# Kernel optimization log

Measured on AMD Instinct MI355X. Metric: run time of the kernel, lower is better.

The kernel has to match this reference:

```python
import jax, jax.numpy as jnp
import numpy as np

N = 100000      # num nodes
E = 1600000     # num edges (avg degree 16)
IN = 128        # input_dim
D = 32          # output_dim per head
H = 4           # heads
ALPHA = 0.2     # LeakyReLU slope


def setup_inputs() -> dict:
    key = jax.random.key(0)
    k1, k2, k3, k4, k5 = jax.random.split(key, 5)
    X = jax.random.normal(k1, (N, IN), dtype=jnp.float32)
    # fc weights, xavier-like scale (bias=False in the module)
    W0 = jax.random.normal(k2, (H * D, IN), dtype=jnp.float32) * (1.0 / np.sqrt(IN))
    W1 = jax.random.normal(k3, (H * D, IN), dtype=jnp.float32) * (1.0 / np.sqrt(IN))
    a0 = jax.random.normal(k4, (H, 1, D), dtype=jnp.float32) * (1.0 / np.sqrt(D))
    deg = E // N
    # CSR rows expanded to sorted segment ids: every node has exactly `deg` out-edges
    edge_src = jnp.repeat(jnp.arange(N, dtype=jnp.int32), deg)
    column_index = jax.random.randint(k5, (E,), 0, N, dtype=jnp.int32)
    return {"X": X, "W0": W0, "W1": W1, "a0": a0,
            "edge_src": edge_src, "column_index": column_index}


def _leaky_relu(x):
    return jnp.where(x > 0, x, ALPHA * x)


def reference(X, W0, W1, a0, edge_src, column_index):
    # Linear projections, split per head: [H, N, D]
    X0 = _leaky_relu(X @ W0.T).reshape(N, H, D).transpose(1, 0, 2)
    X1 = _leaky_relu(X @ W1.T).reshape(N, H, D).transpose(1, 0, 2)
    a = a0[:, 0, :]                                    # [H, D]
    # SDDMM: att[h,e] = a[h] . (X0[h,src(e)] + X1[h,dst(e)])
    s0 = jnp.einsum('hnd,hd->hn', X0, a)               # [H, N]
    s1 = jnp.einsum('hnd,hd->hn', X1, a)
    att = s0[:, edge_src] + s1[:, column_index]        # [H, E]
    # per-head global min-max normalization, then exp (module's softmax surrogate)
    mx = jnp.max(att, axis=1, keepdims=True)
    mn = jnp.min(att, axis=1, keepdims=True)
    att = jnp.exp((att - mn) / (mx - mn))
    # sparse row-sum (softmax denominator): [N, H]
    rows_sum = jax.ops.segment_sum(att.T, edge_src, num_segments=N)
    # SpMM: aggregate neighbor features weighted by att -> [N, H, D]
    msg = att.T[:, :, None] * X1[:, column_index, :].transpose(1, 0, 2)  # [E, H, D]
    h_prime = jax.ops.segment_sum(msg, edge_src, num_segments=N)
    return h_prime / rows_sum[:, :, None]
```

## Files before the change

kernel.cpp:

```cpp
#include <hip/hip_runtime.h>
#include <hip/hip_bf16.h>
#include <stdint.h>

#define NN 100000
#define EE 1600000
#define ALPHA 0.2f
#define MM_BLOCKS 1563

typedef __bf16 bf16_t;
typedef __bf16 bf16x8 __attribute__((ext_vector_type(8)));
typedef __bf16 bf16x4 __attribute__((ext_vector_type(4)));
typedef float fx4 __attribute__((ext_vector_type(4)));


__global__ __launch_bounds__(512) void wconv_kernel(
    const float* __restrict__ W0, const float* __restrict__ W1,
    uint4* __restrict__ Wtab)
{
  const int task = blockIdx.x * 512 + threadIdx.x;
  if (task >= 4096) return;
  const int sct = task >> 8, sks = (task >> 6) & 3, sl = task & 63;
  const int r  = sct * 16 + (sl & 15);
  const int c0 = (sks * 4 + (sl >> 4)) * 8;
  const float* src = (r < 128 ? W0 + (size_t)r * 128 : W1 + (size_t)(r - 128) * 128) + c0;
  const fx4 wa = *(const fx4*)src;
  const fx4 wb = *(const fx4*)(src + 4);
  bf16x8 wf;
  wf[0] = (bf16_t)wa[0]; wf[1] = (bf16_t)wa[1];
  wf[2] = (bf16_t)wa[2]; wf[3] = (bf16_t)wa[3];
  wf[4] = (bf16_t)wb[0]; wf[5] = (bf16_t)wb[1];
  wf[6] = (bf16_t)wb[2]; wf[7] = (bf16_t)wb[3];
  Wtab[task] = __builtin_bit_cast(uint4, wf);
}

#define GEMM_BLOCKS 391
__global__ __launch_bounds__(512) void gemm_kernel(
    const float* __restrict__ X, const uint4* __restrict__ Wtab,
    const float* __restrict__ a0,
    bf16_t* __restrict__ F1, float* __restrict__ s0g, float* __restrict__ s1g)
{
  __shared__ uint4 lw[4096];
  const int tid  = threadIdx.x;
  const int wv   = tid >> 6;
  const int lane = tid & 63;
  const int col  = lane & 15;
  const int quad = lane >> 4;

#pragma unroll
  for (int i = 0; i < 8; ++i) {
    const int task = i * 512 + tid;
    __builtin_amdgcn_global_load_lds(
        (const __attribute__((address_space(1))) uint32_t*)(Wtab + task),
        (__attribute__((address_space(3))) uint32_t*)(&lw[task]), 16, 0, 0);
  }
  __syncthreads();

#pragma unroll 1
  for (int tt = 0; tt < 2; ++tt) {
    const int tile = blockIdx.x * 8 + wv + tt * (GEMM_BLOCKS * 8);
    if (tile >= (NN / 16)) continue;
    const int n0   = tile * 16;
    const int node = n0 + col;

    fx4 acc[16];
#pragma unroll
    for (int c = 0; c < 16; ++c) {
      acc[c][0] = 0.f; acc[c][1] = 0.f; acc[c][2] = 0.f; acc[c][3] = 0.f;
    }

    const float* xrow = X + (size_t)node * 128 + quad * 8;
#pragma unroll
    for (int ks = 0; ks < 4; ++ks) {
      fx4 xa = *(const fx4*)(xrow + ks * 32);
      fx4 xb = *(const fx4*)(xrow + ks * 32 + 4);
      bf16x8 xf;
      xf[0] = (bf16_t)xa[0]; xf[1] = (bf16_t)xa[1];
      xf[2] = (bf16_t)xa[2]; xf[3] = (bf16_t)xa[3];
      xf[4] = (bf16_t)xb[0]; xf[5] = (bf16_t)xb[1];
      xf[6] = (bf16_t)xb[2]; xf[7] = (bf16_t)xb[3];
#pragma unroll
      for (int ct = 0; ct < 16; ++ct) {
        const uint4 w4 = lw[(ct * 4 + ks) * 64 + lane];
        const bf16x8 wf = __builtin_bit_cast(bf16x8, w4);
        acc[ct] = __builtin_amdgcn_mfma_f32_16x16x32_bf16(wf, xf, acc[ct], 0, 0, 0);
      }
    }

    float sdot[8];
#pragma unroll
    for (int s = 0; s < 8; ++s) sdot[s] = 0.f;

#pragma unroll
    for (int ct = 0; ct < 16; ++ct) {
      const fx4 av = *(const fx4*)(a0 + (ct & 7) * 16 + quad * 4);
#pragma unroll
      for (int r = 0; r < 4; ++r) {
        float v = acc[ct][r];
        v = v > 0.f ? v : ALPHA * v;
        acc[ct][r] = v;
        sdot[ct >> 1] += v * av[r];
      }
      if (ct >= 8) {
        bf16x4 p;
        p[0] = (bf16_t)acc[ct][0]; p[1] = (bf16_t)acc[ct][1];
        p[2] = (bf16_t)acc[ct][2]; p[3] = (bf16_t)acc[ct][3];
        *(bf16x4*)(F1 + (size_t)node * 128 + (ct - 8) * 16 + quad * 4) = p;
      }
    }

#pragma unroll
    for (int s = 0; s < 8; ++s) {
      sdot[s] += __shfl_xor(sdot[s], 16);
      sdot[s] += __shfl_xor(sdot[s], 32);
    }
    if (quad == 0) {
      fx4 r0, r1;
      r0[0] = sdot[0]; r0[1] = sdot[1]; r0[2] = sdot[2]; r0[3] = sdot[3];
      r1[0] = sdot[4]; r1[1] = sdot[5]; r1[2] = sdot[6]; r1[3] = sdot[7];
      *(fx4*)(s0g + (size_t)node * 4) = r0;
      *(fx4*)(s1g + (size_t)node * 4) = r1;
    }
  }
}

__global__ __launch_bounds__(256) void minmax1_kernel(
    const int* __restrict__ cidx, const float* __restrict__ s0g,
    const float* __restrict__ s1g, float* __restrict__ partial)
{
  __shared__ float s_red[4][8];
  const int t = blockIdx.x * 256 + threadIdx.x;
  fx4 mx, mn;
#pragma unroll
  for (int h = 0; h < 4; ++h) { mx[h] = -1e30f; mn[h] = 1e30f; }
  if (t < EE / 4) {
    const int node = t >> 2;
    const fx4 s0v = *(const fx4*)(s0g + (size_t)node * 4);
    const int4 c4 = ((const int4*)cidx)[t];
    const int cc[4] = {c4.x, c4.y, c4.z, c4.w};
#pragma unroll
    for (int j = 0; j < 4; ++j) {
      const fx4 s1v = *(const fx4*)(s1g + (size_t)cc[j] * 4);
#pragma unroll
      for (int h = 0; h < 4; ++h) {
        const float att = s0v[h] + s1v[h];
        mx[h] = fmaxf(mx[h], att);
        mn[h] = fminf(mn[h], att);
      }
    }
  }
#pragma unroll
  for (int off = 1; off < 64; off <<= 1) {
#pragma unroll
    for (int h = 0; h < 4; ++h) {
      mx[h] = fmaxf(mx[h], __shfl_xor(mx[h], off));
      mn[h] = fminf(mn[h], __shfl_xor(mn[h], off));
    }
  }
  const int wv = threadIdx.x >> 6;
  if ((threadIdx.x & 63) == 0) {
#pragma unroll
    for (int h = 0; h < 4; ++h) {
      s_red[wv][h] = mx[h];
      s_red[wv][4 + h] = mn[h];
    }
  }
  __syncthreads();
  if (threadIdx.x < 8) {
    const int s = threadIdx.x;
    float v = s_red[0][s];
    if (s < 4) { v = fmaxf(v, s_red[1][s]); v = fmaxf(v, s_red[2][s]); v = fmaxf(v, s_red[3][s]); }
    else       { v = fminf(v, s_red[1][s]); v = fminf(v, s_red[2][s]); v = fminf(v, s_red[3][s]); }
    partial[blockIdx.x * 8 + s] = v;
  }
}

__global__ __launch_bounds__(256) void minmax2_kernel(
    const float* __restrict__ partial, float* __restrict__ mm)
{
  __shared__ float s_red[4][8];
  fx4 mx, mn;
#pragma unroll
  for (int h = 0; h < 4; ++h) { mx[h] = -1e30f; mn[h] = 1e30f; }
  for (int g = threadIdx.x; g < MM_BLOCKS; g += 256) {
    const fx4 p0 = *(const fx4*)(partial + g * 8);
    const fx4 p1 = *(const fx4*)(partial + g * 8 + 4);
#pragma unroll
    for (int h = 0; h < 4; ++h) {
      mx[h] = fmaxf(mx[h], p0[h]);
      mn[h] = fminf(mn[h], p1[h]);
    }
  }
#pragma unroll
  for (int off = 1; off < 64; off <<= 1) {
#pragma unroll
    for (int h = 0; h < 4; ++h) {
      mx[h] = fmaxf(mx[h], __shfl_xor(mx[h], off));
      mn[h] = fminf(mn[h], __shfl_xor(mn[h], off));
    }
  }
  const int wv = threadIdx.x >> 6;
  if ((threadIdx.x & 63) == 0) {
#pragma unroll
    for (int h = 0; h < 4; ++h) {
      s_red[wv][h] = mx[h];
      s_red[wv][4 + h] = mn[h];
    }
  }
  __syncthreads();
  if (threadIdx.x < 8) {
    const int s = threadIdx.x;
    float v = s_red[0][s];
    if (s < 4) { v = fmaxf(v, s_red[1][s]); v = fmaxf(v, s_red[2][s]); v = fmaxf(v, s_red[3][s]); }
    else       { v = fminf(v, s_red[1][s]); v = fminf(v, s_red[2][s]); v = fminf(v, s_red[3][s]); }
    mm[s] = v;
  }
}

__global__ __launch_bounds__(256) void aggregate_kernel(
    const int* __restrict__ cidx, const float* __restrict__ s0g,
    const float* __restrict__ s1g, const bf16_t* __restrict__ F1,
    const float* __restrict__ mm, float* __restrict__ out)
{
  const int t = blockIdx.x * 256 + threadIdx.x;
  const int node = t >> 4;
  if (node >= NN) return;
  const int sub = t & 15;
  const int h = sub >> 2;
  const float mxv = mm[h];
  const float mnv = mm[4 + h];
  const float scale = 1.f / (mxv - mnv);
  const float s0v = s0g[node * 4 + h];
  float a_[8] = {0.f, 0.f, 0.f, 0.f, 0.f, 0.f, 0.f, 0.f};
  float wsum = 0.f;

  const int4* ce4 = (const int4*)(cidx + (size_t)node * 16);
  const int4 c01 = ce4[0], c23 = ce4[1], c45 = ce4[2], c67 = ce4[3];
  const int cc[16] = {c01.x, c01.y, c01.z, c01.w, c23.x, c23.y, c23.z, c23.w,
                      c45.x, c45.y, c45.z, c45.w, c67.x, c67.y, c67.z, c67.w};

  float s1v[16];
  bf16x8 f[16];
#pragma unroll
  for (int j = 0; j < 16; ++j) {
    const int c = cc[j];
    s1v[j] = s1g[(size_t)c * 4 + h];
    f[j] = *(const bf16x8*)(F1 + (size_t)c * 128 + sub * 8);
  }
  __builtin_amdgcn_sched_barrier(0);

#pragma unroll
  for (int j = 0; j < 16; ++j) {
    const float w = __expf((s0v + s1v[j] - mnv) * scale);
    wsum += w;
#pragma unroll
    for (int k = 0; k < 8; ++k) a_[k] += w * (float)f[j][k];
  }

  const float inv = 1.f / wsum;
  fx4 r0, r1;
#pragma unroll
  for (int j = 0; j < 4; ++j) { r0[j] = a_[j] * inv; r1[j] = a_[4 + j] * inv; }
  float* op = out + (size_t)node * 128 + sub * 8;
  *(fx4*)op = r0;
  *(fx4*)(op + 4) = r1;
}

extern "C" void kernel_launch(void* const* d_in, const int* in_sizes, int n_in,
                              void* d_out, int out_size, void* d_ws, size_t ws_size,
                              hipStream_t stream)
{
  const float* X   = (const float*)d_in[0];
  const float* W0  = (const float*)d_in[1];
  const float* W1  = (const float*)d_in[2];
  const float* a0  = (const float*)d_in[3];
  const int* cidx  = (const int*)d_in[5];
  char* ws = (char*)d_ws;
  uint4*    Wtab    = (uint4*)ws;
  bf16_t*   F1      = (bf16_t*)(ws + 65536);
  float*    s0g     = (float*)(ws + 25665536);
  float*    s1g     = (float*)(ws + 27265536);
  float*    mm      = (float*)(ws + 28865536);
  float*    partial = (float*)(ws + 28865600);
  float*    out     = (float*)d_out;

  wconv_kernel<<<8, 512, 0, stream>>>(W0, W1, Wtab);
  gemm_kernel<<<GEMM_BLOCKS, 512, 0, stream>>>(X, Wtab, a0, F1, s0g, s1g);
  minmax1_kernel<<<MM_BLOCKS, 256, 0, stream>>>(cidx, s0g, s1g, partial);
  minmax2_kernel<<<1, 256, 0, stream>>>(partial, mm);
  aggregate_kernel<<<6250, 256, 0, stream>>>(cidx, s0g, s1g, F1, mm, out);
}
```

Measured before the change: 212.2 us.

## Fold final min-max reduction into aggregate kernel and drop minmax2 launch

Removes the single-block minmax2 kernel. Each aggregate block now redundantly reduces the 391 per-block partials into shared memory before doing its own work. The first-stage min-max kernel uses 1024-thread blocks, so there are fewer partials to reduce. The GEMM kernel launches 782 blocks with one tile per wave instead of looping twice over tiles. The aim is to cut a serial single-block launch and its dependency bubble, at the cost of 6250 blocks each re-reading about 12 KB of partials.

```diff
diff --git a/kernel.cpp b/kernel.cpp
--- a/kernel.cpp
+++ b/kernel.cpp
@@ -5,7 +5,7 @@
 #define NN 100000
 #define EE 1600000
 #define ALPHA 0.2f
-#define MM_BLOCKS 1563
+#define MM1_BLOCKS 391
 
 typedef __bf16 bf16_t;
 typedef __bf16 bf16x8 __attribute__((ext_vector_type(8)));
@@ -33,7 +33,6 @@
   Wtab[task] = __builtin_bit_cast(uint4, wf);
 }
 
-#define GEMM_BLOCKS 391
 __global__ __launch_bounds__(512) void gemm_kernel(
     const float* __restrict__ X, const uint4* __restrict__ Wtab,
     const float* __restrict__ a0,
@@ -55,80 +54,77 @@
   }
   __syncthreads();
 
-#pragma unroll 1
-  for (int tt = 0; tt < 2; ++tt) {
-    const int tile = blockIdx.x * 8 + wv + tt * (GEMM_BLOCKS * 8);
-    if (tile >= (NN / 16)) continue;
-    const int n0   = tile * 16;
-    const int node = n0 + col;
-
-    fx4 acc[16];
-#pragma unroll
-    for (int c = 0; c < 16; ++c) {
-      acc[c][0] = 0.f; acc[c][1] = 0.f; acc[c][2] = 0.f; acc[c][3] = 0.f;
-    }
-
-    const float* xrow = X + (size_t)node * 128 + quad * 8;
-#pragma unroll
-    for (int ks = 0; ks < 4; ++ks) {
-      fx4 xa = *(const fx4*)(xrow + ks * 32);
-      fx4 xb = *(const fx4*)(xrow + ks * 32 + 4);
-      bf16x8 xf;
-      xf[0] = (bf16_t)xa[0]; xf[1] = (bf16_t)xa[1];
-      xf[2] = (bf16_t)xa[2]; xf[3] = (bf16_t)xa[3];
-      xf[4] = (bf16_t)xb[0]; xf[5] = (bf16_t)xb[1];
-      xf[6] = (bf16_t)xb[2]; xf[7] = (bf16_t)xb[3];
-#pragma unroll
-      for (int ct = 0; ct < 16; ++ct) {
-        const uint4 w4 = lw[(ct * 4 + ks) * 64 + lane];
-        const bf16x8 wf = __builtin_bit_cast(bf16x8, w4);
-        acc[ct] = __builtin_amdgcn_mfma_f32_16x16x32_bf16(wf, xf, acc[ct], 0, 0, 0);
-      }
-    }
-
-    float sdot[8];
-#pragma unroll
-    for (int s = 0; s < 8; ++s) sdot[s] = 0.f;
-
+  const int tile = blockIdx.x * 8 + wv;
+  if (tile >= (NN / 16)) return;
+  const int n0   = tile * 16;
+  const int node = n0 + col;
+
+  fx4 acc[16];
+#pragma unroll
+  for (int c = 0; c < 16; ++c) {
+    acc[c][0] = 0.f; acc[c][1] = 0.f; acc[c][2] = 0.f; acc[c][3] = 0.f;
+  }
+
+  const float* xrow = X + (size_t)node * 128 + quad * 8;
+#pragma unroll
+  for (int ks = 0; ks < 4; ++ks) {
+    fx4 xa = *(const fx4*)(xrow + ks * 32);
+    fx4 xb = *(const fx4*)(xrow + ks * 32 + 4);
+    bf16x8 xf;
+    xf[0] = (bf16_t)xa[0]; xf[1] = (bf16_t)xa[1];
+    xf[2] = (bf16_t)xa[2]; xf[3] = (bf16_t)xa[3];
+    xf[4] = (bf16_t)xb[0]; xf[5] = (bf16_t)xb[1];
+    xf[6] = (bf16_t)xb[2]; xf[7] = (bf16_t)xb[3];
 #pragma unroll
     for (int ct = 0; ct < 16; ++ct) {
-      const fx4 av = *(const fx4*)(a0 + (ct & 7) * 16 + quad * 4);
-#pragma unroll
-      for (int r = 0; r < 4; ++r) {
-        float v = acc[ct][r];
-        v = v > 0.f ? v : ALPHA * v;
-        acc[ct][r] = v;
-        sdot[ct >> 1] += v * av[r];
-      }
-      if (ct >= 8) {
-        bf16x4 p;
-        p[0] = (bf16_t)acc[ct][0]; p[1] = (bf16_t)acc[ct][1];
-        p[2] = (bf16_t)acc[ct][2]; p[3] = (bf16_t)acc[ct][3];
-        *(bf16x4*)(F1 + (size_t)node * 128 + (ct - 8) * 16 + quad * 4) = p;
-      }
-    }
-
-#pragma unroll
-    for (int s = 0; s < 8; ++s) {
-      sdot[s] += __shfl_xor(sdot[s], 16);
-      sdot[s] += __shfl_xor(sdot[s], 32);
-    }
-    if (quad == 0) {
-      fx4 r0, r1;
-      r0[0] = sdot[0]; r0[1] = sdot[1]; r0[2] = sdot[2]; r0[3] = sdot[3];
-      r1[0] = sdot[4]; r1[1] = sdot[5]; r1[2] = sdot[6]; r1[3] = sdot[7];
-      *(fx4*)(s0g + (size_t)node * 4) = r0;
-      *(fx4*)(s1g + (size_t)node * 4) = r1;
-    }
-  }
-}
-
-__global__ __launch_bounds__(256) void minmax1_kernel(
+      const uint4 w4 = lw[(ct * 4 + ks) * 64 + lane];
+      const bf16x8 wf = __builtin_bit_cast(bf16x8, w4);
+      acc[ct] = __builtin_amdgcn_mfma_f32_16x16x32_bf16(wf, xf, acc[ct], 0, 0, 0);
+    }
+  }
+
+  float sdot[8];
+#pragma unroll
+  for (int s = 0; s < 8; ++s) sdot[s] = 0.f;
+
+#pragma unroll
+  for (int ct = 0; ct < 16; ++ct) {
+    const fx4 av = *(const fx4*)(a0 + (ct & 7) * 16 + quad * 4);
+#pragma unroll
+    for (int r = 0; r < 4; ++r) {
+      float v = acc[ct][r];
+      v = v > 0.f ? v : ALPHA * v;
+      acc[ct][r] = v;
+      sdot[ct >> 1] += v * av[r];
+    }
+    if (ct >= 8) {
+      bf16x4 p;
+      p[0] = (bf16_t)acc[ct][0]; p[1] = (bf16_t)acc[ct][1];
+      p[2] = (bf16_t)acc[ct][2]; p[3] = (bf16_t)acc[ct][3];
+      *(bf16x4*)(F1 + (size_t)node * 128 + (ct - 8) * 16 + quad * 4) = p;
+    }
+  }
+
+#pragma unroll
+  for (int s = 0; s < 8; ++s) {
+    sdot[s] += __shfl_xor(sdot[s], 16);
+    sdot[s] += __shfl_xor(sdot[s], 32);
+  }
+  if (quad == 0) {
+    fx4 r0, r1;
+    r0[0] = sdot[0]; r0[1] = sdot[1]; r0[2] = sdot[2]; r0[3] = sdot[3];
+    r1[0] = sdot[4]; r1[1] = sdot[5]; r1[2] = sdot[6]; r1[3] = sdot[7];
+    *(fx4*)(s0g + (size_t)node * 4) = r0;
+    *(fx4*)(s1g + (size_t)node * 4) = r1;
+  }
+}
+
+__global__ __launch_bounds__(1024) void minmax1_kernel(
     const int* __restrict__ cidx, const float* __restrict__ s0g,
     const float* __restrict__ s1g, float* __restrict__ partial)
 {
-  __shared__ float s_red[4][8];
-  const int t = blockIdx.x * 256 + threadIdx.x;
+  __shared__ float s_red[16][8];
+  const int t = blockIdx.x * 1024 + threadIdx.x;
   fx4 mx, mn;
 #pragma unroll
   for (int h = 0; h < 4; ++h) { mx[h] = -1e30f; mn[h] = 1e30f; }
@@ -168,66 +164,71 @@
   if (threadIdx.x < 8) {
     const int s = threadIdx.x;
     float v = s_red[0][s];
-    if (s < 4) { v = fmaxf(v, s_red[1][s]); v = fmaxf(v, s_red[2][s]); v = fmaxf(v, s_red[3][s]); }
-    else       { v = fminf(v, s_red[1][s]); v = fminf(v, s_red[2][s]); v = fminf(v, s_red[3][s]); }
+    if (s < 4) {
+#pragma unroll
+      for (int w = 1; w < 16; ++w) v = fmaxf(v, s_red[w][s]);
+    } else {
+#pragma unroll
+      for (int w = 1; w < 16; ++w) v = fminf(v, s_red[w][s]);
+    }
     partial[blockIdx.x * 8 + s] = v;
-  }
-}
-
-__global__ __launch_bounds__(256) void minmax2_kernel(
-    const float* __restrict__ partial, float* __restrict__ mm)
-{
-  __shared__ float s_red[4][8];
-  fx4 mx, mn;
-#pragma unroll
-  for (int h = 0; h < 4; ++h) { mx[h] = -1e30f; mn[h] = 1e30f; }
-  for (int g = threadIdx.x; g < MM_BLOCKS; g += 256) {
-    const fx4 p0 = *(const fx4*)(partial + g * 8);
-    const fx4 p1 = *(const fx4*)(partial + g * 8 + 4);
-#pragma unroll
-    for (int h = 0; h < 4; ++h) {
-      mx[h] = fmaxf(mx[h], p0[h]);
-      mn[h] = fminf(mn[h], p1[h]);
-    }
-  }
-#pragma unroll
-  for (int off = 1; off < 64; off <<= 1) {
-#pragma unroll
-    for (int h = 0; h < 4; ++h) {
-      mx[h] = fmaxf(mx[h], __shfl_xor(mx[h], off));
-      mn[h] = fminf(mn[h], __shfl_xor(mn[h], off));
-    }
-  }
-  const int wv = threadIdx.x >> 6;
-  if ((threadIdx.x & 63) == 0) {
-#pragma unroll
-    for (int h = 0; h < 4; ++h) {
-      s_red[wv][h] = mx[h];
-      s_red[wv][4 + h] = mn[h];
-    }
-  }
-  __syncthreads();
-  if (threadIdx.x < 8) {
-    const int s = threadIdx.x;
-    float v = s_red[0][s];
-    if (s < 4) { v = fmaxf(v, s_red[1][s]); v = fmaxf(v, s_red[2][s]); v = fmaxf(v, s_red[3][s]); }
-    else       { v = fminf(v, s_red[1][s]); v = fminf(v, s_red[2][s]); v = fminf(v, s_red[3][s]); }
-    mm[s] = v;
   }
 }
 
 __global__ __launch_bounds__(256) void aggregate_kernel(
     const int* __restrict__ cidx, const float* __restrict__ s0g,
     const float* __restrict__ s1g, const bf16_t* __restrict__ F1,
-    const float* __restrict__ mm, float* __restrict__ out)
-{
+    const float* __restrict__ partial, float* __restrict__ out)
+{
+  __shared__ float s_mm[8];
+  __shared__ float s_red[4][8];
+  {
+    fx4 mx, mn;
+#pragma unroll
+    for (int h = 0; h < 4; ++h) { mx[h] = -1e30f; mn[h] = 1e30f; }
+    for (int g = threadIdx.x; g < MM1_BLOCKS; g += 256) {
+      const fx4 p0 = *(const fx4*)(partial + g * 8);
+      const fx4 p1 = *(const fx4*)(partial + g * 8 + 4);
+#pragma unroll
+      for (int h = 0; h < 4; ++h) {
+        mx[h] = fmaxf(mx[h], p0[h]);
+        mn[h] = fminf(mn[h], p1[h]);
+      }
+    }
+#pragma unroll
+    for (int off = 1; off < 64; off <<= 1) {
+#pragma unroll
+      for (int h = 0; h < 4; ++h) {
+        mx[h] = fmaxf(mx[h], __shfl_xor(mx[h], off));
+        mn[h] = fminf(mn[h], __shfl_xor(mn[h], off));
+      }
+    }
+    const int wv = threadIdx.x >> 6;
+    if ((threadIdx.x & 63) == 0) {
+#pragma unroll
+      for (int h = 0; h < 4; ++h) {
+        s_red[wv][h] = mx[h];
+        s_red[wv][4 + h] = mn[h];
+      }
+    }
+    __syncthreads();
+    if (threadIdx.x < 8) {
+      const int s = threadIdx.x;
+      float v = s_red[0][s];
+      if (s < 4) { v = fmaxf(v, s_red[1][s]); v = fmaxf(v, s_red[2][s]); v = fmaxf(v, s_red[3][s]); }
+      else       { v = fminf(v, s_red[1][s]); v = fminf(v, s_red[2][s]); v = fminf(v, s_red[3][s]); }
+      s_mm[s] = v;
+    }
+    __syncthreads();
+  }
+
   const int t = blockIdx.x * 256 + threadIdx.x;
   const int node = t >> 4;
   if (node >= NN) return;
   const int sub = t & 15;
   const int h = sub >> 2;
-  const float mxv = mm[h];
-  const float mnv = mm[4 + h];
+  const float mxv = s_mm[h];
+  const float mnv = s_mm[4 + h];
   const float scale = 1.f / (mxv - mnv);
   const float s0v = s0g[node * 4 + h];
   float a_[8] = {0.f, 0.f, 0.f, 0.f, 0.f, 0.f, 0.f, 0.f};
@@ -279,13 +280,11 @@
   bf16_t*   F1      = (bf16_t*)(ws + 65536);
   float*    s0g     = (float*)(ws + 25665536);
   float*    s1g     = (float*)(ws + 27265536);
-  float*    mm      = (float*)(ws + 28865536);
   float*    partial = (float*)(ws + 28865600);
   float*    out     = (float*)d_out;
 
   wconv_kernel<<<8, 512, 0, stream>>>(W0, W1, Wtab);
-  gemm_kernel<<<GEMM_BLOCKS, 512, 0, stream>>>(X, Wtab, a0, F1, s0g, s1g);
-  minmax1_kernel<<<MM_BLOCKS, 256, 0, stream>>>(cidx, s0g, s1g, partial);
-  minmax2_kernel<<<1, 256, 0, stream>>>(partial, mm);
-  aggregate_kernel<<<6250, 256, 0, stream>>>(cidx, s0g, s1g, F1, mm, out);
-}
+  gemm_kernel<<<782, 512, 0, stream>>>(X, Wtab, a0, F1, s0g, s1g);
+  minmax1_kernel<<<MM1_BLOCKS, 1024, 0, stream>>>(cidx, s0g, s1g, partial);
+  aggregate_kernel<<<6250, 256, 0, stream>>>(cidx, s0g, s1g, F1, partial, out);
+}
```

After: 209.7 us. Within noise of the previous version (-1.2%).
